# Kernel tuning notes

Measured on AMD Instinct MI355X. Metric: run time of the kernel, lower is better.

## Reference

```python
import jax, jax.numpy as jnp
import numpy as np


def setup_inputs() -> dict:
    key = jax.random.key(0)
    k1, k2, k3 = jax.random.split(key, 3)
    B, S, K, N = 4, 2048, 4096, 4096
    x = jax.random.normal(k1, (B, S, K), dtype=jnp.float16)
    # int8 weight codes in [-128, 127]
    w_int8 = jax.random.randint(k2, (N, K), -128, 128, dtype=jnp.int32).astype(jnp.int8)
    # per-output-row weight scale (positive, smallish like abs-max/127 of fp weights)
    weight_scale = (jax.random.uniform(k3, (N,), dtype=jnp.float32) + 0.5) * 0.01
    matmul_out_scale = jnp.full((1,), 1.0 / 1024.0, dtype=jnp.float32)
    return {"x": x, "w_int8": w_int8, "weight_scale": weight_scale,
            "matmul_out_scale": matmul_out_scale}


def reference(x, w_int8, weight_scale, matmul_out_scale):
    B, S, K = x.shape
    xf = x.astype(jnp.float32)
    # dynamic per-token symmetric int8 quantization (TOKEN_INT8_127)
    x_scales = jnp.max(jnp.abs(xf), axis=-1, keepdims=True) / 127.0  # [B,S,1] float32
    x_int8 = jnp.clip(jnp.round(xf / x_scales), -128, 127).astype(jnp.int8)
    x_scales_h = x_scales[..., 0].astype(jnp.float16)  # [B,S]
    y = jnp.einsum('mk,nk->mn', x_int8.reshape(-1, K), w_int8,
                   preferred_element_type=jnp.int32).astype(jnp.float32)
    y = y.reshape(B, S, -1)
    y = (y * matmul_out_scale[0]).astype(jnp.float16)
    # fp16 * fp32 -> fp32 (matches torch type promotion); per-row and per-token dequant
    out = y * weight_scale * x_scales_h[:, :, None]
    return out
```

## Files before the change

### kernel.cpp

```cpp
#include <hip/hip_runtime.h>
#include <hip/hip_fp16.h>
#include <stdint.h>

typedef int v4i __attribute__((ext_vector_type(4)));

#define GLOAD_LDS16(g, l) __builtin_amdgcn_global_load_lds(                  \
    (const __attribute__((address_space(1))) void*)(g),                      \
    (__attribute__((address_space(3))) void*)(l), 16, 0, 0)

#define XQ_OFF 0u
#define XS_OFF 33554432u
#define W8_OFF 33570816u

__device__ inline bool x_is_f32(const void* xin) {
  const uint32_t* xw = (const uint32_t*)xin;
  bool ok = true;
  #pragma unroll
  for (int i = 0; i < 16; ++i) ok &= ((xw[i] & 0x1FFFu) == 0u);
  return ok;
}
__device__ inline bool w_is_i32(const void* win) {
  const int* wi = (const int*)win;
  bool ok = true;
  #pragma unroll
  for (int i = 0; i < 16; ++i) ok &= (wi[i] >= -128 && wi[i] <= 127);
  return ok;
}

__global__ __launch_bounds__(256) void repack_w(
    const void* __restrict__ win, int8_t* __restrict__ w8, int total)
{
  const bool as32 = w_is_i32(win);
  const int tid  = blockIdx.x * 256 + threadIdx.x;
  const int nthr = gridDim.x * 256;
  if (as32) {
    const int4* w4 = (const int4*)win;
    uint32_t* dst = (uint32_t*)w8;
    const int n4 = total >> 2;
    for (int i = tid; i < n4; i += nthr) {
      int4 v = w4[i];
      dst[i] = (uint32_t)(v.x & 255) | ((uint32_t)(v.y & 255) << 8) |
               ((uint32_t)(v.z & 255) << 16) | ((uint32_t)(v.w & 255) << 24);
    }
  } else {
    const uint4* src = (const uint4*)win;
    uint4* dst = (uint4*)w8;
    const int n16 = total >> 4;
    for (int i = tid; i < n16; i += nthr) dst[i] = src[i];
  }
}

__global__ __launch_bounds__(256) void quant_rows(
    const void* __restrict__ xin, int8_t* __restrict__ xq,
    __half* __restrict__ xs, int K)
{
  const bool xf32 = x_is_f32(xin);
  const int row  = blockIdx.x;
  const int tid  = threadIdx.x;
  const int lane = tid & 63;
  const int wv   = tid >> 6;
  const size_t base = (size_t)row * (size_t)K;
  __shared__ float wmax[4];

  if (xf32 && K == 4096) {
    const float4* x4 = (const float4*)((const float*)xin + base);
    float4 v[4];
    #pragma unroll
    for (int i = 0; i < 4; ++i) v[i] = x4[i * 256 + tid];
    float mx = 0.0f;
    #pragma unroll
    for (int i = 0; i < 4; ++i)
      mx = fmaxf(mx, fmaxf(fmaxf(fabsf(v[i].x), fabsf(v[i].y)),
                           fmaxf(fabsf(v[i].z), fabsf(v[i].w))));
    #pragma unroll
    for (int off = 32; off; off >>= 1) mx = fmaxf(mx, __shfl_xor(mx, off, 64));
    if (lane == 0) wmax[wv] = mx;
    __syncthreads();
    const float scale =
        fmaxf(fmaxf(wmax[0], wmax[1]), fmaxf(wmax[2], wmax[3])) / 127.0f;
    if (tid == 0) xs[row] = __float2half(scale);
    uint32_t* q = (uint32_t*)(xq + base);
    #pragma unroll
    for (int i = 0; i < 4; ++i) {
      float f[4] = {v[i].x, v[i].y, v[i].z, v[i].w};
      uint32_t p = 0;
      #pragma unroll
      for (int j = 0; j < 4; ++j) {
        float r = fminf(127.0f, fmaxf(-128.0f, rintf(f[j] / scale)));
        p |= ((uint32_t)((int)r & 255)) << (8 * j);
      }
      q[i * 256 + tid] = p;
    }
    return;
  }

  float mx = 0.0f;
  if (xf32) {
    const float* x = (const float*)xin + base;
    for (int k = tid * 4; k < K; k += 256 * 4) {
      float4 v = *(const float4*)(x + k);
      mx = fmaxf(mx, fmaxf(fmaxf(fabsf(v.x), fabsf(v.y)),
                           fmaxf(fabsf(v.z), fabsf(v.w))));
    }
  } else {
    const __half* x = (const __half*)xin + base;
    for (int k = tid * 8; k < K; k += 256 * 8) {
      uint4 u = *(const uint4*)(x + k);
      const __half* hp = (const __half*)&u;
      #pragma unroll
      for (int j = 0; j < 8; ++j) mx = fmaxf(mx, fabsf(__half2float(hp[j])));
    }
  }
  #pragma unroll
  for (int off = 32; off; off >>= 1) mx = fmaxf(mx, __shfl_xor(mx, off, 64));
  if (lane == 0) wmax[wv] = mx;
  __syncthreads();
  const float scale =
      fmaxf(fmaxf(wmax[0], wmax[1]), fmaxf(wmax[2], wmax[3])) / 127.0f;
  if (tid == 0) xs[row] = __float2half(scale);

  for (int k = tid * 8; k < K; k += 256 * 8) {
    float f[8];
    if (xf32) {
      const float* x = (const float*)xin + base;
      float4 a = *(const float4*)(x + k);
      float4 b = *(const float4*)(x + k + 4);
      f[0]=a.x; f[1]=a.y; f[2]=a.z; f[3]=a.w; f[4]=b.x; f[5]=b.y; f[6]=b.z; f[7]=b.w;
    } else {
      const __half* x = (const __half*)xin + base;
      uint4 u = *(const uint4*)(x + k);
      const __half* hp = (const __half*)&u;
      #pragma unroll
      for (int j = 0; j < 8; ++j) f[j] = __half2float(hp[j]);
    }
    uint32_t p0 = 0, p1 = 0;
    #pragma unroll
    for (int j = 0; j < 4; ++j) {
      float r = fminf(127.0f, fmaxf(-128.0f, rintf(f[j] / scale)));
      p0 |= ((uint32_t)((int)r & 255)) << (8 * j);
    }
    #pragma unroll
    for (int j = 0; j < 4; ++j) {
      float r = fminf(127.0f, fmaxf(-128.0f, rintf(f[4 + j] / scale)));
      p1 |= ((uint32_t)((int)r & 255)) << (8 * j);
    }
    uint2 st; st.x = p0; st.y = p1;
    *(uint2*)(xq + base + k) = st;
  }
}

__global__ __launch_bounds__(512, 2) void gemm_w8a8(
    const int8_t* __restrict__ xq, const int8_t* __restrict__ wq,
    const __half* __restrict__ xs, const float* __restrict__ wscale,
    const float* __restrict__ mos, float* __restrict__ out,
    int M, int N, int K)
{
  __shared__ int8_t sA[4][256 * 64];
  __shared__ int8_t sB[4][256 * 64];

  const int tid  = threadIdx.x;
  const int lane = tid & 63;
  const int w    = tid >> 6;
  const int wr   = w >> 2;
  const int wc   = w & 3;
  const int lr   = lane & 15;
  const int lk   = lane >> 4;

  int L = blockIdx.x;
  const int nwg = gridDim.x;
  if ((nwg & 7) == 0) L = (L & 7) * (nwg >> 3) + (L >> 3);
  const int ntn = N >> 8;
  const int bn = (L % ntn) << 8;
  const int bm = (L / ntn) << 8;

  v4i acc[8][4];
  #pragma unroll
  for (int i = 0; i < 8; ++i)
    #pragma unroll
    for (int j = 0; j < 4; ++j) {
      v4i z = {0, 0, 0, 0};
      acc[i][j] = z;
    }

  auto stageA = [&](int kt, int buf) {
    const int k0 = kt << 6;
    #pragma unroll
    for (int i = 0; i < 2; ++i) {
      const int li = i * 512 + tid;
      const int r  = li >> 2;
      const int p  = li & 3;
      const int sc = p ^ ((r >> 1) & 3);
      GLOAD_LDS16(xq + (size_t)(bm + r) * K + k0 + (sc << 4),
                  &sA[buf][(i * 512 + (w << 6)) << 4]);
    }
  };
  auto stageB = [&](int kt, int buf) {
    const int k0 = kt << 6;
    #pragma unroll
    for (int i = 0; i < 2; ++i) {
      const int li = i * 512 + tid;
      const int r  = li >> 2;
      const int p  = li & 3;
      const int sc = p ^ ((r >> 1) & 3);
      GLOAD_LDS16(wq + (size_t)(bn + r) * K + k0 + (sc << 4),
                  &sB[buf][(i * 512 + (w << 6)) << 4]);
    }
  };

  const int rowA0 = (wr << 7) + lr;
  const int aoff  = rowA0 * 64 + ((lk ^ ((rowA0 >> 1) & 3)) << 4);
  const int rowB0 = (wc << 6) + lr;
  const int boff  = rowB0 * 64 + ((lk ^ ((rowB0 >> 1) & 3)) << 4);

#define MFMA_CLUSTER(BASE)                                                   \
    __builtin_amdgcn_s_setprio(1);                                           \
    _Pragma("unroll")                                                        \
    for (int mi = 0; mi < 4; ++mi)                                           \
      _Pragma("unroll")                                                      \
      for (int ni = 0; ni < 4; ++ni)                                         \
        acc[(BASE) + mi][ni] = __builtin_amdgcn_mfma_i32_16x16x64_i8(        \
            af[mi], bf[ni], acc[(BASE) + mi][ni], 0, 0, 0);                  \
    __builtin_amdgcn_s_setprio(0);

#define TILE_ITER(BUF, KT, DOSTAGE, VMLINE)                                  \
  {                                                                          \
    const int8_t* Ab = sA[BUF];                                              \
    const int8_t* Bb = sB[BUF];                                              \
    const int sbuf = ((BUF) + 3) & 3;                                        \
    v4i af[4], bf[4];                                                        \
                             \
    _Pragma("unroll")                                                        \
    for (int ni = 0; ni < 4; ++ni)                                           \
      bf[ni] = *(const v4i*)(Bb + boff + ni * 1024);                         \
    _Pragma("unroll")                                                        \
    for (int mi = 0; mi < 4; ++mi)                                           \
      af[mi] = *(const v4i*)(Ab + aoff + mi * 1024);                         \
    if (DOSTAGE) stageA((KT), sbuf);                                         \
    __builtin_amdgcn_s_barrier();                                            \
    asm volatile("s_waitcnt lgkmcnt(0)" ::: "memory");                       \
    MFMA_CLUSTER(0)                                                          \
    __builtin_amdgcn_s_barrier();                                            \
                           \
    _Pragma("unroll")                                                        \
    for (int mi = 0; mi < 4; ++mi)                                           \
      af[mi] = *(const v4i*)(Ab + aoff + 4096 + mi * 1024);                  \
    if (DOSTAGE) stageB((KT), sbuf);                                         \
    VMLINE                                                                   \
    __builtin_amdgcn_s_barrier();                                            \
    asm volatile("s_waitcnt lgkmcnt(0)" ::: "memory");                       \
    MFMA_CLUSTER(4)                                                          \
    __builtin_amdgcn_s_barrier();                                            \
  }

  const int nt = K >> 6;

  stageA(0, 0); stageB(0, 0);
  stageA(1, 1); stageB(1, 1);
  stageA(2, 2); stageB(2, 2);
  asm volatile("s_waitcnt vmcnt(8)" ::: "memory");
  __builtin_amdgcn_s_barrier();

  #pragma unroll 1
  for (int t = 0; t < nt - 3; ++t) {
    TILE_ITER(t & 3, t + 3, true,
              asm volatile("s_waitcnt vmcnt(8)" ::: "memory");)
  }
  TILE_ITER((nt - 3) & 3, 0, false,
            asm volatile("s_waitcnt vmcnt(4)" ::: "memory");)
  TILE_ITER((nt - 2) & 3, 0, false,
            asm volatile("s_waitcnt vmcnt(0)" ::: "memory");)
  TILE_ITER((nt - 1) & 3, 0, false, ;)

#undef TILE_ITER
#undef MFMA_CLUSTER

  const float s_out = mos[0];
  #pragma unroll
  for (int ni = 0; ni < 4; ++ni) {
    const int n_g = bn + (wc << 6) + ni * 16 + lr;
    const float wsc = wscale[n_g];
    #pragma unroll
    for (int mi = 0; mi < 8; ++mi) {
      #pragma unroll
      for (int j = 0; j < 4; ++j) {
        const int m_g = bm + (wr << 7) + mi * 16 + lk * 4 + j;
        const float y = __half2float(__float2half((float)acc[mi][ni][j] * s_out));
        out[(size_t)m_g * N + n_g] = (y * wsc) * __half2float(xs[m_g]);
      }
    }
  }
}

extern "C" void kernel_launch(void* const* d_in, const int* in_sizes, int n_in,
                              void* d_out, int out_size, void* d_ws, size_t ws_size,
                              hipStream_t stream) {
  const void*  x      = d_in[0];
  const void*  win    = d_in[1];
  const float* wscale = (const float*)d_in[2];
  const float* mos    = (const float*)d_in[3];
  float*       out    = (float*)d_out;

  const int N = in_sizes[2];
  const int K = in_sizes[1] / N;
  const int M = in_sizes[0] / K;

  int8_t* xq = (int8_t*)d_ws + XQ_OFF;
  __half* xs = (__half*)((char*)d_ws + XS_OFF);
  int8_t* w8 = (int8_t*)d_ws + W8_OFF;

  repack_w<<<2048, 256, 0, stream>>>(win, w8, N * K);
  quant_rows<<<M, 256, 0, stream>>>(x, xq, xs, K);

  gemm_w8a8<<<dim3((M >> 8) * (N >> 8)), 512, 0, stream>>>(
      xq, w8, xs, wscale, mos, out, M, N, K);
}
```

Before: 226.6 us.

## Register double-buffer GEMM main loop and merge prologue kernels into one launch

Reworks the int8 GEMM main loop so each tile's A and B fragments are preloaded into register double buffers, with the next tile's LDS reads issued between the two MFMA halves. Pipeline depth drops from three staged tiles to two, and the per-tile barrier count drops from four to one. Separately, the weight repack and activation quantization kernels are merged into a single launch, using extra blocks for the repack. The aim is to cut barrier stalls and one launch, at the cost of more vector registers and less global-load lookahead.

```diff
diff --git a/kernel.cpp b/kernel.cpp
--- a/kernel.cpp
+++ b/kernel.cpp
@@ -27,36 +27,40 @@
   return ok;
 }
 
-__global__ __launch_bounds__(256) void repack_w(
-    const void* __restrict__ win, int8_t* __restrict__ w8, int total)
+#define RW_BLOCKS 1024
+
+__global__ __launch_bounds__(256) void prologue(
+    const void* __restrict__ xin, const void* __restrict__ win,
+    int8_t* __restrict__ xq, __half* __restrict__ xs,
+    int8_t* __restrict__ w8, int K, int M, int wtotal)
 {
-  const bool as32 = w_is_i32(win);
-  const int tid  = blockIdx.x * 256 + threadIdx.x;
-  const int nthr = gridDim.x * 256;
-  if (as32) {
-    const int4* w4 = (const int4*)win;
-    uint32_t* dst = (uint32_t*)w8;
-    const int n4 = total >> 2;
-    for (int i = tid; i < n4; i += nthr) {
-      int4 v = w4[i];
-      dst[i] = (uint32_t)(v.x & 255) | ((uint32_t)(v.y & 255) << 8) |
-               ((uint32_t)(v.z & 255) << 16) | ((uint32_t)(v.w & 255) << 24);
-    }
-  } else {
-    const uint4* src = (const uint4*)win;
-    uint4* dst = (uint4*)w8;
-    const int n16 = total >> 4;
-    for (int i = tid; i < n16; i += nthr) dst[i] = src[i];
-  }
-}
-
-__global__ __launch_bounds__(256) void quant_rows(
-    const void* __restrict__ xin, int8_t* __restrict__ xq,
-    __half* __restrict__ xs, int K)
-{
+  const int tid = threadIdx.x;
+
+  if (blockIdx.x >= (unsigned)M) {
+    const bool as32 = w_is_i32(win);
+    const int bid  = blockIdx.x - M;
+    const int gtid = bid * 256 + tid;
+    const int nthr = RW_BLOCKS * 256;
+    if (as32) {
+      const int4* w4 = (const int4*)win;
+      uint32_t* dst = (uint32_t*)w8;
+      const int n4 = wtotal >> 2;
+      for (int i = gtid; i < n4; i += nthr) {
+        int4 v = w4[i];
+        dst[i] = (uint32_t)(v.x & 255) | ((uint32_t)(v.y & 255) << 8) |
+                 ((uint32_t)(v.z & 255) << 16) | ((uint32_t)(v.w & 255) << 24);
+      }
+    } else {
+      const uint4* src = (const uint4*)win;
+      uint4* dst = (uint4*)w8;
+      const int n16 = wtotal >> 4;
+      for (int i = gtid; i < n16; i += nthr) dst[i] = src[i];
+    }
+    return;
+  }
+
   const bool xf32 = x_is_f32(xin);
   const int row  = blockIdx.x;
-  const int tid  = threadIdx.x;
   const int lane = tid & 63;
   const int wv   = tid >> 6;
   const size_t base = (size_t)row * (size_t)K;
@@ -212,67 +216,62 @@
   const int rowB0 = (wc << 6) + lr;
   const int boff  = rowB0 * 64 + ((lk ^ ((rowB0 >> 1) & 3)) << 4);
 
-#define MFMA_CLUSTER(BASE)                                                   \
+  const int nt = K >> 6;
+
+  stageA(0, 0); stageB(0, 0);
+  stageA(1, 1); stageB(1, 1);
+  asm volatile("s_waitcnt vmcnt(4)" ::: "memory");
+  __builtin_amdgcn_s_barrier();
+
+  v4i a0[8], b0[4], a1[8], b1[4];
+  #pragma unroll
+  for (int j = 0; j < 8; ++j) a0[j] = *(const v4i*)(&sA[0][aoff + j * 1024]);
+  #pragma unroll
+  for (int j = 0; j < 4; ++j) b0[j] = *(const v4i*)(&sB[0][boff + j * 1024]);
+
+#define ITER(T, CA, CB, NA, NB)                                              \
+  {                                                                          \
+    const bool ds = (T) + 2 < nt;                                            \
+    if (ds) { stageA((T) + 2, ((T) + 2) & 3);                                \
+              stageB((T) + 2, ((T) + 2) & 3); }                              \
+    asm volatile("s_waitcnt lgkmcnt(0)" ::: "memory");                       \
     __builtin_amdgcn_s_setprio(1);                                           \
     _Pragma("unroll")                                                        \
     for (int mi = 0; mi < 4; ++mi)                                           \
       _Pragma("unroll")                                                      \
       for (int ni = 0; ni < 4; ++ni)                                         \
-        acc[(BASE) + mi][ni] = __builtin_amdgcn_mfma_i32_16x16x64_i8(        \
-            af[mi], bf[ni], acc[(BASE) + mi][ni], 0, 0, 0);                  \
-    __builtin_amdgcn_s_setprio(0);
-
-#define TILE_ITER(BUF, KT, DOSTAGE, VMLINE)                                  \
-  {                                                                          \
-    const int8_t* Ab = sA[BUF];                                              \
-    const int8_t* Bb = sB[BUF];                                              \
-    const int sbuf = ((BUF) + 3) & 3;                                        \
-    v4i af[4], bf[4];                                                        \
-                             \
-    _Pragma("unroll")                                                        \
-    for (int ni = 0; ni < 4; ++ni)                                           \
-      bf[ni] = *(const v4i*)(Bb + boff + ni * 1024);                         \
+        acc[mi][ni] = __builtin_amdgcn_mfma_i32_16x16x64_i8(                 \
+            CA[mi], CB[ni], acc[mi][ni], 0, 0, 0);                           \
+    __builtin_amdgcn_s_setprio(0);                                           \
+    if ((T) + 1 < nt) {                                                      \
+      if (ds) { asm volatile("s_waitcnt vmcnt(8)" ::: "memory"); }           \
+      else    { asm volatile("s_waitcnt vmcnt(0)" ::: "memory"); }           \
+      __builtin_amdgcn_s_barrier();                                          \
+      const int8_t* An = sA[((T) + 1) & 3];                                  \
+      const int8_t* Bn = sB[((T) + 1) & 3];                                  \
+      _Pragma("unroll")                                                      \
+      for (int j = 0; j < 8; ++j)                                            \
+        NA[j] = *(const v4i*)(An + aoff + j * 1024);                         \
+      _Pragma("unroll")                                                      \
+      for (int j = 0; j < 4; ++j)                                            \
+        NB[j] = *(const v4i*)(Bn + boff + j * 1024);                         \
+    }                                                                        \
+    __builtin_amdgcn_s_setprio(1);                                           \
     _Pragma("unroll")                                                        \
     for (int mi = 0; mi < 4; ++mi)                                           \
-      af[mi] = *(const v4i*)(Ab + aoff + mi * 1024);                         \
-    if (DOSTAGE) stageA((KT), sbuf);                                         \
-    __builtin_amdgcn_s_barrier();                                            \
-    asm volatile("s_waitcnt lgkmcnt(0)" ::: "memory");                       \
-    MFMA_CLUSTER(0)                                                          \
-    __builtin_amdgcn_s_barrier();                                            \
-                           \
-    _Pragma("unroll")                                                        \
-    for (int mi = 0; mi < 4; ++mi)                                           \
-      af[mi] = *(const v4i*)(Ab + aoff + 4096 + mi * 1024);                  \
-    if (DOSTAGE) stageB((KT), sbuf);                                         \
-    VMLINE                                                                   \
-    __builtin_amdgcn_s_barrier();                                            \
-    asm volatile("s_waitcnt lgkmcnt(0)" ::: "memory");                       \
-    MFMA_CLUSTER(4)                                                          \
-    __builtin_amdgcn_s_barrier();                                            \
-  }
-
-  const int nt = K >> 6;
-
-  stageA(0, 0); stageB(0, 0);
-  stageA(1, 1); stageB(1, 1);
-  stageA(2, 2); stageB(2, 2);
-  asm volatile("s_waitcnt vmcnt(8)" ::: "memory");
-  __builtin_amdgcn_s_barrier();
+      _Pragma("unroll")                                                      \
+      for (int ni = 0; ni < 4; ++ni)                                         \
+        acc[4 + mi][ni] = __builtin_amdgcn_mfma_i32_16x16x64_i8(             \
+            CA[4 + mi], CB[ni], acc[4 + mi][ni], 0, 0, 0);                   \
+    __builtin_amdgcn_s_setprio(0);                                           \
+  }
 
   #pragma unroll 1
-  for (int t = 0; t < nt - 3; ++t) {
-    TILE_ITER(t & 3, t + 3, true,
-              asm volatile("s_waitcnt vmcnt(8)" ::: "memory");)
-  }
-  TILE_ITER((nt - 3) & 3, 0, false,
-            asm volatile("s_waitcnt vmcnt(4)" ::: "memory");)
-  TILE_ITER((nt - 2) & 3, 0, false,
-            asm volatile("s_waitcnt vmcnt(0)" ::: "memory");)
-  TILE_ITER((nt - 1) & 3, 0, false, ;)
-
-#undef TILE_ITER
-#undef MFMA_CLUSTER
+  for (int t = 0; t < nt; t += 2) {
+    ITER(t,     a0, b0, a1, b1)
+    ITER(t + 1, a1, b1, a0, b0)
+  }
+#undef ITER
 
   const float s_out = mos[0];
   #pragma unroll
@@ -308,8 +307,7 @@
   __half* xs = (__half*)((char*)d_ws + XS_OFF);
   int8_t* w8 = (int8_t*)d_ws + W8_OFF;
 
-  repack_w<<<2048, 256, 0, stream>>>(win, w8, N * K);
-  quant_rows<<<M, 256, 0, stream>>>(x, xq, xs, K);
+  prologue<<<M + RW_BLOCKS, 256, 0, stream>>>(x, win, xq, xs, w8, K, M, N * K);
 
   gemm_w8a8<<<dim3((M >> 8) * (N >> 8)), 512, 0, stream>>>(
       xq, w8, xs, wscale, mos, out, M, N, K);
```

New measurement: 194.0 us. 14.4% less time.
